# Kernel tuning notes

Hardware: AMD Instinct MI355X
Metric: run time of the kernel (lower is better)

The kernel has to match this reference:

```python
import math
import jax, jax.numpy as jnp
import numpy as np

B, C_IN, C_OUT, K, STYLE_DIM, H, W = 8, 512, 512, 3, 512, 64, 64
EPS = 1e-8

def setup_inputs() -> dict:
    key = jax.random.key(0)
    k1, k2, k3, k4 = jax.random.split(key, 4)
    inp = {
        "input": jax.random.normal(k1, (B, C_IN, H, W), dtype=jnp.float32),
        "style": jax.random.normal(k2, (B, STYLE_DIM), dtype=jnp.float32),
        # learned params
        "weight": jax.random.normal(k3, (1, C_OUT, C_IN, K, K), dtype=jnp.float32),
        "mod_weight": jax.random.normal(k4, (C_IN, STYLE_DIM), dtype=jnp.float32),  # EqualLinear weight (lr_mul=1)
        "mod_bias": jnp.ones((C_IN,), dtype=jnp.float32),  # bias_init=1
    }
    return inp

def reference(input, style, weight, mod_weight, mod_bias):
    batch, in_ch, h, w = input.shape
    out_ch, ksize = weight.shape[1], weight.shape[-1]
    # EqualLinear modulation: scale = 1/sqrt(style_dim), lr_mul = 1
    mod_scale = 1.0 / math.sqrt(mod_weight.shape[1])
    s = style @ (mod_weight * mod_scale).T + mod_bias  # [B, C_in]
    # modulate weights per sample
    conv_scale = 1.0 / math.sqrt(in_ch * ksize * ksize)
    wmod = conv_scale * weight * s[:, None, :, None, None]  # [B, O, C, k, k]
    # demodulate
    demod = jax.lax.rsqrt(jnp.sum(wmod * wmod, axis=(2, 3, 4)) + EPS)  # [B, O]
    wmod = wmod * demod[:, :, None, None, None]
    # grouped conv with groups = batch
    wflat = wmod.reshape(batch * out_ch, in_ch, ksize, ksize)
    xflat = input.reshape(1, batch * in_ch, h, w)
    pad = ksize // 2
    out = jax.lax.conv_general_dilated(
        xflat, wflat,
        window_strides=(1, 1),
        padding=[(pad, pad), (pad, pad)],
        dimension_numbers=("NCHW", "OIHW", "NCHW"),
        feature_group_count=batch,
    )
    return out.reshape(batch, out_ch, h, w)
```

## Files before the change

kernel.cpp:

```cpp
#include <hip/hip_runtime.h>


typedef __bf16 bf16x8 __attribute__((ext_vector_type(8)));
typedef float f32x16 __attribute__((ext_vector_type(16)));

#define AS1 __attribute__((address_space(1)))
#define AS3 __attribute__((address_space(3)))
#define SB __builtin_amdgcn_sched_barrier(0)

__device__ __forceinline__ unsigned short f2bf(float f) {
  union { float f; unsigned int u; } v; v.f = f;
  unsigned int u = v.u;
  return (unsigned short)((u + 0x7fffu + ((u >> 16) & 1u)) >> 16);
}

__device__ __forceinline__ float dot8(float4 a0, float4 a1, float4 b0, float4 b1) {
  return a0.x*b0.x + a0.y*b0.y + a0.z*b0.z + a0.w*b0.w +
         a1.x*b1.x + a1.y*b1.y + a1.z*b1.z + a1.w*b1.w;
}

__global__ __launch_bounds__(256) void k_mod(
    const float* __restrict__ style, const float* __restrict__ mw,
    const float* __restrict__ mb, float* __restrict__ s,
    float* __restrict__ zp) {
  if (blockIdx.x == 0) {
    zp[threadIdx.x] = 0.f; zp[256 + threadIdx.x] = 0.f;
    zp[512 + threadIdx.x] = 0.f; zp[768 + threadIdx.x] = 0.f;
  }
  int wv = blockIdx.x * 4 + (threadIdx.x >> 6);
  int lane = threadIdx.x & 63;
  int t0 = wv * 4;
#pragma unroll
  for (int j = 0; j < 4; ++j) {
    int t = t0 + j, b = t >> 9, c = t & 511;
    const float4* mp = (const float4*)(mw + (size_t)c * 512 + lane * 8);
    const float4* sp = (const float4*)(style + (size_t)b * 512 + lane * 8);
    float p = dot8(mp[0], mp[1], sp[0], sp[1]);
#pragma unroll
    for (int off = 32; off; off >>= 1) p += __shfl_xor(p, off);
    if (lane == 0) s[t] = p * 0.04419417382415922f + mb[c];
  }
}

__global__ __launch_bounds__(256) void k_wprep(
    const float* __restrict__ w, float* __restrict__ wsq,
    unsigned short* __restrict__ wbf2) {
  __shared__ float wl[4608];
  int o = blockIdx.x;
  int t = threadIdx.x;
  const float* wp = w + (size_t)o * 4608;
  for (int i = t; i < 4608; i += 256) wl[i] = wp[i];
  __syncthreads();
  int c0 = t * 2;
  float q0 = 0.f, q1 = 0.f;
  unsigned int rr[9];
#pragma unroll
  for (int k = 0; k < 9; ++k) {
    float v0 = wl[c0 * 9 + k], v1 = wl[c0 * 9 + 9 + k];
    q0 += v0 * v0; q1 += v1 * v1;
    rr[k] = (unsigned int)f2bf(v0) | ((unsigned int)f2bf(v1) << 16);
  }
  *(float2*)&wsq[o * 512 + c0] = make_float2(q0, q1);
#pragma unroll
  for (int k = 0; k < 9; ++k) {
    size_t idx = ((size_t)(k * 32 + (c0 >> 4)) * 512 + o) * 16 +
                 ((c0 >> 3) & 1) * 8 + (c0 & 7);
    *(unsigned int*)&wbf2[idx] = rr[k];
  }
}

__global__ __launch_bounds__(256) void k_scale(
    const float* __restrict__ wsq, const float* __restrict__ s,
    float* __restrict__ scale) {
  int o = blockIdx.x * 4 + (threadIdx.x >> 6);
  int lane = threadIdx.x & 63;
  const float4* wp = (const float4*)(wsq + (size_t)o * 512 + lane * 8);
  float4 w0 = wp[0], w1 = wp[1];
  const float cs = 0.014731391274719739f;
#pragma unroll
  for (int b = 0; b < 8; ++b) {
    const float4* sp = (const float4*)(s + (size_t)b * 512 + lane * 8);
    float4 s0 = sp[0], s1 = sp[1];
    s0.x *= s0.x; s0.y *= s0.y; s0.z *= s0.z; s0.w *= s0.w;
    s1.x *= s1.x; s1.y *= s1.y; s1.z *= s1.z; s1.w *= s1.w;
    float p = dot8(w0, w1, s0, s1);
#pragma unroll
    for (int off = 32; off; off >>= 1) p += __shfl_xor(p, off);
    if (lane == 0) scale[b * 512 + o] = cs * rsqrtf(cs * cs * p + 1e-8f);
  }
}

__global__ void k_xt(const float* __restrict__ x, const float* __restrict__ s,
                     unsigned short* __restrict__ xt) {
  __shared__ __align__(16) unsigned short tile[64 * 65 * 8];
  int bid = blockIdx.x;
  int b = bid >> 6, y = bid & 63;
  int t = threadIdx.x;
  int co = t >> 3, xo = t & 7;
  const float* xbase = x + ((size_t)(b * 512 + co * 8) * 64 + y) * 64 + xo * 8;
  float4 v[8][2];
#pragma unroll
  for (int j = 0; j < 8; ++j) {
    v[j][0] = *(const float4*)(xbase + (size_t)j * 4096);
    v[j][1] = *(const float4*)(xbase + (size_t)j * 4096 + 4);
  }
  float sv[8];
#pragma unroll
  for (int j = 0; j < 8; ++j) sv[j] = s[b * 512 + co * 8 + j];
#pragma unroll
  for (int k = 0; k < 8; ++k) {
    unsigned short r[8];
#pragma unroll
    for (int j = 0; j < 8; ++j) {
      float f = (k < 4) ? ((const float*)&v[j][0])[k & 3]
                        : ((const float*)&v[j][1])[k & 3];
      r[j] = f2bf(f * sv[j]);
    }
    int xr = xo * 8 + k;
    int unit = xr * 65 + (co ^ xr);
    *(ulonglong2*)&tile[unit * 8] = *(ulonglong2*)r;
  }
  __syncthreads();
  unsigned short* obase = xt + ((size_t)(b * 64 + y) * 64) * 512;
#pragma unroll
  for (int i = 0; i < 8; ++i) {
    int unit_o = i * 512 + t;
    int xr = unit_o >> 6, cor = unit_o & 63;
    int unit = xr * 65 + (cor ^ xr);
    *(ulonglong2*)&obase[(size_t)unit_o * 8] = *(const ulonglong2*)&tile[unit * 8];
  }
}

#define XISS 20
#define BUFU  12288

__global__ __launch_bounds__(512, 2) void k_conv(
    const unsigned short* __restrict__ xt, const unsigned short* __restrict__ wbf2,
    const float* __restrict__ scale, const float* __restrict__ zp,
    float* __restrict__ out) {
  __shared__ __align__(16) unsigned short lds[4 * BUFU];

  int bid = blockIdx.x;
  int b = bid & 7;
  int rest = bid >> 3;
  int ob = rest & 3;
  int rest2 = rest >> 2;
  int yg = rest2 & 3;
  int xg = rest2 >> 2;

  int tid = threadIdx.x;
  int wid = tid >> 6;
  int wo = wid & 1, wyy = wid >> 1;
  int lane = tid & 63, ln31 = lane & 31, hi = lane >> 5;

  const char* srcp[3];
  const char* xglob = (const char*)(xt + (size_t)b * 64 * 64 * 512);
#pragma unroll
  for (int i = 0; i < 3; ++i) {
    int is = wid + i * 8;
    const char* p = (const char*)zp;
    if (is < XISS) {
      int e = is * 64 + lane;
      int chunk = e / 612;
      int rem = e - chunk * 612;
      int row = rem / 34;
      int xi = rem - row * 34;
      int y = yg * 16 + row - 1, x = xg * 32 + xi - 1;
      bool ok = (chunk < 2) && (y >= 0) && (y < 64) && (x >= 0) && (x < 64);
      if (ok) p = xglob + 2 * ((y * 64 + x) * 512 + chunk * 8);
    }
    srcp[i] = p;
  }

  const char* aw0 = (const char*)wbf2 +
      2 * (((size_t)(ob * 128 + wo * 64 + ln31)) * 16 + hi * 8);
  const char* aw1 = aw0 + 1024;

  f32x16 acc[8];
#pragma unroll
  for (int i = 0; i < 8; ++i)
    acc[i] = (f32x16){0,0,0,0,0,0,0,0,0,0,0,0,0,0,0,0};

  auto STAGE = [&](int bufu, bool real) {
#pragma unroll
    for (int i = 0; i < 3; ++i) {
      const char* src = real ? srcp[i] : (const char*)zp;
      __builtin_amdgcn_global_load_lds(
          (const AS1 void*)src,
          (AS3 void*)&lds[bufu + (wid + i * 8) * 512], 16, 0, 0);
      srcp[i] += 32;
    }
  };

  auto LOADA = [&](int kx, int aoff, bf16x8* A) {
#pragma unroll
    for (int ky = 0; ky < 3; ++ky) {
      int tap = ky * 3 + kx;
      A[ky * 2]     = *(const bf16x8*)(aw0 + (size_t)tap * 524288 + aoff);
      A[ky * 2 + 1] = *(const bf16x8*)(aw1 + (size_t)tap * 524288 + aoff);
    }
  };

  auto LOADB = [&](const unsigned short* Xbp, int kx, bf16x8* bv) {
#pragma unroll
    for (int rr = 0; rr < 6; ++rr)
      bv[rr] = *(const bf16x8*)&Xbp[(rr * 34 + kx) * 8];
  };

  auto MFK = [&](const bf16x8* av, const bf16x8* bv) {
    __builtin_amdgcn_s_setprio(1);
#pragma unroll
    for (int ky = 0; ky < 3; ++ky) {
#pragma unroll
      for (int ry = 0; ry < 4; ++ry) {
        acc[ry] = __builtin_amdgcn_mfma_f32_32x32x16_bf16(
            av[ky * 2], bv[ry + ky], acc[ry], 0, 0, 0);
        acc[4 + ry] = __builtin_amdgcn_mfma_f32_32x32x16_bf16(
            av[ky * 2 + 1], bv[ry + ky], acc[4 + ry], 0, 0, 0);
      }
    }
    __builtin_amdgcn_s_setprio(0);
  };

  auto PHASE = [&](const unsigned short* Xbp, int stageBufU, bool real,
                   bf16x8* Su, bf16x8* Sl, int aoff) {
    bf16x8 bv[6];
    LOADB(Xbp, 0, bv);
    STAGE(stageBufU, real);
    LOADA(1, aoff, Sl);
    MFK(Su, bv);
    LOADB(Xbp, 1, bv);
    LOADA(2, aoff, Su);
    MFK(Sl, bv);
    LOADB(Xbp, 2, bv);
    LOADA(0, aoff + 16384, Sl);
    MFK(Su, bv);
    asm volatile("s_waitcnt vmcnt(9)" ::: "memory");
    __builtin_amdgcn_s_barrier();
    SB;
  };

  const unsigned short* Xw = &lds[(hi * 612 + wyy * 136 + ln31) * 8];
  const unsigned short* Xq0 = Xw;
  const unsigned short* Xq1 = Xw + BUFU;
  const unsigned short* Xq2 = Xw + 2 * BUFU;
  const unsigned short* Xq3 = Xw + 3 * BUFU;

  bf16x8 SA[6], SB_[6];

  STAGE(0, true);
  STAGE(BUFU, true);
  LOADA(0, 0, SA);
  asm volatile("s_waitcnt vmcnt(9)" ::: "memory");
  __builtin_amdgcn_s_barrier();
  SB;

  int aoff = 0;
#pragma unroll 1
  for (int t4 = 0; t4 < 8; ++t4) {
    bool r = (t4 < 7);
    PHASE(Xq0, 2 * BUFU, true, SA, SB_, aoff); aoff += 16384;
    PHASE(Xq1, 3 * BUFU, true, SB_, SA, aoff); aoff += 16384;
    PHASE(Xq2, 0,        r,    SA, SB_, aoff); aoff += 16384;
    PHASE(Xq3, 1 * BUFU, r,    SB_, SA, aoff); aoff += 16384;
  }

  const float* scp = scale + b * 512 + ob * 128 + wo * 64;
  float* op = out + (((size_t)(b * 512 + ob * 128 + wo * 64) * 64) +
                     yg * 16 + wyy * 4) * 64 + xg * 32 + ln31;
#pragma unroll
  for (int oh = 0; oh < 2; ++oh) {
#pragma unroll
    for (int ry = 0; ry < 4; ++ry) {
      const f32x16& A = acc[oh * 4 + ry];
#pragma unroll
      for (int reg = 0; reg < 16; ++reg) {
        int orow = (reg & 3) + 8 * (reg >> 2) + hi * 4;
        int ol = oh * 32 + orow;
        op[(size_t)ol * 4096 + ry * 64] = A[reg] * scp[ol];
      }
    }
  }
}

extern "C" void kernel_launch(void* const* d_in, const int* in_sizes, int n_in,
                              void* d_out, int out_size, void* d_ws, size_t ws_size,
                              hipStream_t stream) {
  const float* x     = (const float*)d_in[0];
  const float* style = (const float*)d_in[1];
  const float* w     = (const float*)d_in[2];
  const float* mw    = (const float*)d_in[3];
  const float* mb    = (const float*)d_in[4];
  float* out = (float*)d_out;

  char* ws = (char*)d_ws;
  float* zp    = (float*)ws;
  float* s     = (float*)(ws + 4096);
  float* scale = (float*)(ws + 20480);
  float* wsq   = (float*)(ws + 36864);
  unsigned short* wbf2 = (unsigned short*)(ws + 1085440);
  unsigned short* xt   = (unsigned short*)(ws + 5804032);

  k_mod  <<<256,  256, 0, stream>>>(style, mw, mb, s, zp);
  k_wprep<<<512,  256, 0, stream>>>(w, wsq, wbf2);
  k_scale<<<128,  256, 0, stream>>>(wsq, s, scale);
  k_xt   <<<512,  512, 0, stream>>>(x, s, xt);
  k_conv <<<256,  512, 0, stream>>>(xt, wbf2, scale, zp, out);
}
```

Baseline: 178.0 us.

## Double-buffer 32-channel input stages instead of quad-buffering 16-channel stages

The conv main loop now stages 32 input channels (four chunks) per step into two larger LDS buffers, replacing four smaller 16-channel buffers. This halves the number of barrier-synchronised phases and packs six MFMA groups per barrier instead of three. The cost is less prefetch depth (only one stage ahead), a changed vmcnt wait scheme, and somewhat more LDS per block (80 KB vs 96 KB; actually less), which could expose global-load latency.

```diff
diff --git a/kernel.cpp b/kernel.cpp
--- a/kernel.cpp
+++ b/kernel.cpp
@@ -131,14 +131,13 @@
   }
 }
 
-#define XISS 20
-#define BUFU  12288
+#define BUFU  20480
 
 __global__ __launch_bounds__(512, 2) void k_conv(
     const unsigned short* __restrict__ xt, const unsigned short* __restrict__ wbf2,
     const float* __restrict__ scale, const float* __restrict__ zp,
     float* __restrict__ out) {
-  __shared__ __align__(16) unsigned short lds[4 * BUFU];
+  __shared__ __align__(16) unsigned short lds[2 * BUFU];
 
   int bid = blockIdx.x;
   int b = bid & 7;
@@ -153,23 +152,20 @@
   int wo = wid & 1, wyy = wid >> 1;
   int lane = tid & 63, ln31 = lane & 31, hi = lane >> 5;
 
-  const char* srcp[3];
+  const char* srcp[5];
   const char* xglob = (const char*)(xt + (size_t)b * 64 * 64 * 512);
 #pragma unroll
-  for (int i = 0; i < 3; ++i) {
+  for (int i = 0; i < 5; ++i) {
     int is = wid + i * 8;
-    const char* p = (const char*)zp;
-    if (is < XISS) {
-      int e = is * 64 + lane;
-      int chunk = e / 612;
-      int rem = e - chunk * 612;
-      int row = rem / 34;
-      int xi = rem - row * 34;
-      int y = yg * 16 + row - 1, x = xg * 32 + xi - 1;
-      bool ok = (chunk < 2) && (y >= 0) && (y < 64) && (x >= 0) && (x < 64);
-      if (ok) p = xglob + 2 * ((y * 64 + x) * 512 + chunk * 8);
-    }
-    srcp[i] = p;
+    int e = is * 64 + lane;
+    int chunk = e / 612;
+    int rem = e - chunk * 612;
+    int row = rem / 34;
+    int xi = rem - row * 34;
+    int y = yg * 16 + row - 1, x = xg * 32 + xi - 1;
+    bool ok = (chunk < 4) && (y >= 0) && (y < 64) && (x >= 0) && (x < 64);
+    srcp[i] = ok ? xglob + 2 * ((y * 64 + x) * 512 + chunk * 8)
+                 : (const char*)zp;
   }
 
   const char* aw0 = (const char*)wbf2 +
@@ -181,14 +177,13 @@
   for (int i = 0; i < 8; ++i)
     acc[i] = (f32x16){0,0,0,0,0,0,0,0,0,0,0,0,0,0,0,0};
 
-  auto STAGE = [&](int bufu, bool real) {
-#pragma unroll
-    for (int i = 0; i < 3; ++i) {
-      const char* src = real ? srcp[i] : (const char*)zp;
+  auto STAGE = [&](int bufu) {
+#pragma unroll
+    for (int i = 0; i < 5; ++i) {
       __builtin_amdgcn_global_load_lds(
-          (const AS1 void*)src,
+          (const AS1 void*)srcp[i],
           (AS3 void*)&lds[bufu + (wid + i * 8) * 512], 16, 0, 0);
-      srcp[i] += 32;
+      srcp[i] += 64;
     }
   };
 
@@ -201,10 +196,10 @@
     }
   };
 
-  auto LOADB = [&](const unsigned short* Xbp, int kx, bf16x8* bv) {
+  auto LOADB = [&](const unsigned short* Xbp, int s, int kx, bf16x8* bv) {
 #pragma unroll
     for (int rr = 0; rr < 6; ++rr)
-      bv[rr] = *(const bf16x8*)&Xbp[(rr * 34 + kx) * 8];
+      bv[rr] = *(const bf16x8*)&Xbp[s * 9792 + (rr * 34 + kx) * 8];
   };
 
   auto MFK = [&](const bf16x8* av, const bf16x8* bv) {
@@ -222,47 +217,44 @@
     __builtin_amdgcn_s_setprio(0);
   };
 
-  auto PHASE = [&](const unsigned short* Xbp, int stageBufU, bool real,
-                   bf16x8* Su, bf16x8* Sl, int aoff) {
+  const unsigned short* Xw = &lds[(hi * 612 + wyy * 136 + ln31) * 8];
+
+  bf16x8 S0[6], S1[6];
+
+  STAGE(0);
+  LOADA(0, 0, S0);
+  asm volatile("s_waitcnt vmcnt(6)" ::: "memory");
+  __builtin_amdgcn_s_barrier();
+  SB;
+
+#pragma unroll 1
+  for (int t = 0; t < 16; ++t) {
+    const unsigned short* Xbp = Xw + (t & 1) * BUFU;
+    int sbuf = ((t & 1) ^ 1) * BUFU;
+    int aoff = t * 32768;
     bf16x8 bv[6];
-    LOADB(Xbp, 0, bv);
-    STAGE(stageBufU, real);
-    LOADA(1, aoff, Sl);
-    MFK(Su, bv);
-    LOADB(Xbp, 1, bv);
-    LOADA(2, aoff, Su);
-    MFK(Sl, bv);
-    LOADB(Xbp, 2, bv);
-    LOADA(0, aoff + 16384, Sl);
-    MFK(Su, bv);
-    asm volatile("s_waitcnt vmcnt(9)" ::: "memory");
+    LOADB(Xbp, 0, 0, bv);
+    if (t < 15) STAGE(sbuf);
+    LOADA(1, aoff, S1);
+    MFK(S0, bv);
+    LOADB(Xbp, 0, 1, bv);
+    LOADA(2, aoff, S0);
+    MFK(S1, bv);
+    LOADB(Xbp, 0, 2, bv);
+    LOADA(0, aoff + 16384, S1);
+    MFK(S0, bv);
+    LOADB(Xbp, 1, 0, bv);
+    LOADA(1, aoff + 16384, S0);
+    MFK(S1, bv);
+    LOADB(Xbp, 1, 1, bv);
+    LOADA(2, aoff + 16384, S1);
+    MFK(S0, bv);
+    LOADB(Xbp, 1, 2, bv);
+    if (t < 15) LOADA(0, aoff + 32768, S0);
+    MFK(S1, bv);
+    asm volatile("s_waitcnt vmcnt(36)" ::: "memory");
     __builtin_amdgcn_s_barrier();
     SB;
-  };
-
-  const unsigned short* Xw = &lds[(hi * 612 + wyy * 136 + ln31) * 8];
-  const unsigned short* Xq0 = Xw;
-  const unsigned short* Xq1 = Xw + BUFU;
-  const unsigned short* Xq2 = Xw + 2 * BUFU;
-  const unsigned short* Xq3 = Xw + 3 * BUFU;
-
-  bf16x8 SA[6], SB_[6];
-
-  STAGE(0, true);
-  STAGE(BUFU, true);
-  LOADA(0, 0, SA);
-  asm volatile("s_waitcnt vmcnt(9)" ::: "memory");
-  __builtin_amdgcn_s_barrier();
-  SB;
-
-  int aoff = 0;
-#pragma unroll 1
-  for (int t4 = 0; t4 < 8; ++t4) {
-    bool r = (t4 < 7);
-    PHASE(Xq0, 2 * BUFU, true, SA, SB_, aoff); aoff += 16384;
-    PHASE(Xq1, 3 * BUFU, true, SB_, SA, aoff); aoff += 16384;
-    PHASE(Xq2, 0,        r,    SA, SB_, aoff); aoff += 16384;
-    PHASE(Xq3, 1 * BUFU, r,    SB_, SA, aoff); aoff += 16384;
   }
 
   const float* scp = scale + b * 512 + ob * 128 + wo * 64;
```

Measured after the change: 175.5 us. No clear change (-1.4%).

## Halve conv block tile to 8 rows with 256 threads and 512 blocks

Applied to the files above, without the earlier changes.

The conv kernel now uses blocks of 4 waves, each covering an 8-row by 32-column output tile instead of 16 rows, and launches twice as many blocks. LDS staging buffers are halved, and the pipeline loop is rewritten as a flat 32-step schedule that skips staging and weight prefetch on the final steps instead of loading from a zero page. The explicit vmcnt wait inside each phase is removed. The weight-repack index is simplified to an equivalent form. This should improve occupancy and load balance across CUs, at the cost of more halo rows per output and less weight reuse per block, plus a risk from dropping the per-phase vmcnt wait.

```diff
diff --git a/kernel.cpp b/kernel.cpp
--- a/kernel.cpp
+++ b/kernel.cpp
@@ -63,8 +63,7 @@
   *(float2*)&wsq[o * 512 + c0] = make_float2(q0, q1);
 #pragma unroll
   for (int k = 0; k < 9; ++k) {
-    size_t idx = ((size_t)(k * 32 + (c0 >> 4)) * 512 + o) * 16 +
-                 ((c0 >> 3) & 1) * 8 + (c0 & 7);
+    size_t idx = ((size_t)(k * 32 + (c0 >> 4)) * 512 + o) * 16 + (c0 & 15);
     *(unsigned int*)&wbf2[idx] = rr[k];
   }
 }
@@ -131,10 +130,9 @@
   }
 }
 
-#define XISS 20
-#define BUFU  12288
-
-__global__ __launch_bounds__(512, 2) void k_conv(
+#define BUFU  6144
+
+__global__ __launch_bounds__(256, 2) void k_conv(
     const unsigned short* __restrict__ xt, const unsigned short* __restrict__ wbf2,
     const float* __restrict__ scale, const float* __restrict__ zp,
     float* __restrict__ out) {
@@ -145,8 +143,8 @@
   int rest = bid >> 3;
   int ob = rest & 3;
   int rest2 = rest >> 2;
-  int yg = rest2 & 3;
-  int xg = rest2 >> 2;
+  int yg = rest2 & 7;
+  int xg = rest2 >> 3;
 
   int tid = threadIdx.x;
   int wid = tid >> 6;
@@ -157,15 +155,15 @@
   const char* xglob = (const char*)(xt + (size_t)b * 64 * 64 * 512);
 #pragma unroll
   for (int i = 0; i < 3; ++i) {
-    int is = wid + i * 8;
+    int is = wid + i * 4;
     const char* p = (const char*)zp;
-    if (is < XISS) {
+    if (is < 11) {
       int e = is * 64 + lane;
-      int chunk = e / 612;
-      int rem = e - chunk * 612;
+      int chunk = e / 340;
+      int rem = e - chunk * 340;
       int row = rem / 34;
       int xi = rem - row * 34;
-      int y = yg * 16 + row - 1, x = xg * 32 + xi - 1;
+      int y = yg * 8 + row - 1, x = xg * 32 + xi - 1;
       bool ok = (chunk < 2) && (y >= 0) && (y < 64) && (x >= 0) && (x < 64);
       if (ok) p = xglob + 2 * ((y * 64 + x) * 512 + chunk * 8);
     }
@@ -181,13 +179,12 @@
   for (int i = 0; i < 8; ++i)
     acc[i] = (f32x16){0,0,0,0,0,0,0,0,0,0,0,0,0,0,0,0};
 
-  auto STAGE = [&](int bufu, bool real) {
+  auto STAGE = [&](int bufu) {
 #pragma unroll
     for (int i = 0; i < 3; ++i) {
-      const char* src = real ? srcp[i] : (const char*)zp;
       __builtin_amdgcn_global_load_lds(
-          (const AS1 void*)src,
-          (AS3 void*)&lds[bufu + (wid + i * 8) * 512], 16, 0, 0);
+          (const AS1 void*)srcp[i],
+          (AS3 void*)&lds[bufu + (wid + i * 4) * 512], 16, 0, 0);
       srcp[i] += 32;
     }
   };
@@ -222,52 +219,44 @@
     __builtin_amdgcn_s_setprio(0);
   };
 
-  auto PHASE = [&](const unsigned short* Xbp, int stageBufU, bool real,
-                   bf16x8* Su, bf16x8* Sl, int aoff) {
+  const unsigned short* Xw = &lds[(hi * 340 + wyy * 136 + ln31) * 8];
+
+  bf16x8 S0[6], S1[6];
+
+  STAGE(0);
+  STAGE(BUFU);
+  LOADA(0, 0, S0);
+  asm volatile("s_waitcnt vmcnt(18)" ::: "memory");
+  __builtin_amdgcn_s_barrier();
+  SB;
+
+  auto PHASE = [&](int t, bf16x8* Su, bf16x8* Sl) {
+    const unsigned short* Xbp = Xw + (t & 3) * BUFU;
+    int aoff = t * 16384;
     bf16x8 bv[6];
+    if (t < 30) STAGE(((t + 2) & 3) * BUFU);
     LOADB(Xbp, 0, bv);
-    STAGE(stageBufU, real);
     LOADA(1, aoff, Sl);
     MFK(Su, bv);
     LOADB(Xbp, 1, bv);
     LOADA(2, aoff, Su);
     MFK(Sl, bv);
     LOADB(Xbp, 2, bv);
-    LOADA(0, aoff + 16384, Sl);
+    if (t < 31) LOADA(0, aoff + 16384, Sl);
     MFK(Su, bv);
-    asm volatile("s_waitcnt vmcnt(9)" ::: "memory");
     __builtin_amdgcn_s_barrier();
     SB;
   };
 
-  const unsigned short* Xw = &lds[(hi * 612 + wyy * 136 + ln31) * 8];
-  const unsigned short* Xq0 = Xw;
-  const unsigned short* Xq1 = Xw + BUFU;
-  const unsigned short* Xq2 = Xw + 2 * BUFU;
-  const unsigned short* Xq3 = Xw + 3 * BUFU;
-
-  bf16x8 SA[6], SB_[6];
-
-  STAGE(0, true);
-  STAGE(BUFU, true);
-  LOADA(0, 0, SA);
-  asm volatile("s_waitcnt vmcnt(9)" ::: "memory");
-  __builtin_amdgcn_s_barrier();
-  SB;
-
-  int aoff = 0;
 #pragma unroll 1
-  for (int t4 = 0; t4 < 8; ++t4) {
-    bool r = (t4 < 7);
-    PHASE(Xq0, 2 * BUFU, true, SA, SB_, aoff); aoff += 16384;
-    PHASE(Xq1, 3 * BUFU, true, SB_, SA, aoff); aoff += 16384;
-    PHASE(Xq2, 0,        r,    SA, SB_, aoff); aoff += 16384;
-    PHASE(Xq3, 1 * BUFU, r,    SB_, SA, aoff); aoff += 16384;
+  for (int t = 0; t < 32; t += 2) {
+    PHASE(t, S0, S1);
+    PHASE(t + 1, S1, S0);
   }
 
   const float* scp = scale + b * 512 + ob * 128 + wo * 64;
   float* op = out + (((size_t)(b * 512 + ob * 128 + wo * 64) * 64) +
-                     yg * 16 + wyy * 4) * 64 + xg * 32 + ln31;
+                     yg * 8 + wyy * 4) * 64 + xg * 32 + ln31;
 #pragma unroll
   for (int oh = 0; oh < 2; ++oh) {
 #pragma unroll
@@ -305,5 +294,5 @@
   k_wprep<<<512,  256, 0, stream>>>(w, wsq, wbf2);
   k_scale<<<128,  256, 0, stream>>>(wsq, s, scale);
   k_xt   <<<512,  512, 0, stream>>>(x, s, xt);
-  k_conv <<<256,  512, 0, stream>>>(xt, wbf2, scale, zp, out);
-}
+  k_conv <<<512,  256, 0, stream>>>(xt, wbf2, scale, zp, out);
+}
```

After: 174.9 us. No clear change (-1.7%).
